# Performance work log

Hardware: AMD Instinct MI355X
Metric: run time of the kernel (lower is better)

Reference implementation:

```python
import jax, jax.numpy as jnp
import numpy as np
import itertools

N_INPUTS = 6
N_TERMS = 4
# static rule index table [R, n_inputs], R = n_terms ** n_inputs = 4096
RULE_IDX = np.array(list(itertools.product(range(N_TERMS), repeat=N_INPUTS)), dtype=np.int32)


def setup_inputs() -> dict:
    key = jax.random.key(0)
    k1, k2, k3, k4 = jax.random.split(key, 4)
    B = 32768
    x = jax.random.normal(k1, (B, N_INPUTS), dtype=jnp.float32)
    centers = jax.random.normal(k2, (N_INPUTS, N_TERMS), dtype=jnp.float32)
    sigmas = jax.random.uniform(k3, (N_INPUTS, N_TERMS), dtype=jnp.float32, minval=0.5, maxval=1.5)
    consequents = jax.random.normal(k4, (N_TERMS ** N_INPUTS, N_INPUTS + 1), dtype=jnp.float32)
    return {"x": x, "centers": centers, "sigmas": sigmas, "consequents": consequents}


def reference(x, centers, sigmas, consequents):
    # Gaussian memberships: mu[b, i, t]
    s = jnp.abs(sigmas) + 1e-6                          # [I, T]
    mu = jnp.exp(-((x[:, :, None] - centers[None]) ** 2) / (2.0 * s[None] ** 2))  # [B, I, T]
    # rule firing strengths: product over inputs of selected terms
    idx = jnp.asarray(RULE_IDX.T)                       # [I, R]
    mu_sel = jnp.take_along_axis(mu, idx[None], axis=2)  # [B, I, R]
    w = jnp.prod(mu_sel, axis=1)                        # [B, R]
    w_norm = w / (jnp.sum(w, axis=1, keepdims=True) + 1e-8)
    # consequent outputs: f[b, r] = [x, 1] @ consequents[r]
    x_aug = jnp.concatenate([x, jnp.ones((x.shape[0], 1), dtype=x.dtype)], axis=1)  # [B, I+1]
    f = x_aug @ consequents.T                           # [B, R]
    return jnp.sum(w_norm * f, axis=1, keepdims=True)   # [B, 1]
```

## Files before the change

### kernel.cpp

```cpp
#include <hip/hip_runtime.h>


typedef __attribute__((ext_vector_type(8))) short bf16x8;
typedef __attribute__((ext_vector_type(4))) float f32x4;

#define THREADS 256
#define BPB     64
#define PH_STR  66
#define PTT_STR 65

__device__ __forceinline__ unsigned int bf16rne(float f) {
    unsigned int u = __float_as_uint(f);
    u += 0x7fffu + ((u >> 16) & 1u);
    return u >> 16;
}

__global__ void anfis_prep(const float* __restrict__ cons, uint4* __restrict__ ws) {
    int id = blockIdx.x * blockDim.x + threadIdx.x;
    if (id >= 4096) return;
    int l = id >> 6, n = id & 63;
    const float* src = cons + (n * 64 + l) * 7;
    unsigned int h[8];
#pragma unroll
    for (int j = 0; j < 7; ++j) h[j] = bf16rne(src[j]);
    h[7] = 0;
    uint4 v;
    v.x = h[0] | (h[1] << 16);
    v.y = h[2] | (h[3] << 16);
    v.z = h[4] | (h[5] << 16);
    v.w = h[6] | (h[7] << 16);
    ws[id] = v;
}

__launch_bounds__(THREADS, 4)
__global__ void anfis_mfma(const float* __restrict__ x,
                           const float* __restrict__ centers,
                           const float* __restrict__ sigmas,
                           const uint4* __restrict__ wsC,
                           float* __restrict__ out, int B) {
    __shared__ float  PH[BPB * PH_STR];
    __shared__ float  PTT[64 * PTT_STR];
    __shared__ float4 xs4[BPB * 6 / 4];

    const int tid  = threadIdx.x;
    const int lane = tid & 63;
    const int wv   = tid >> 6;
    const long blockbase = (long)blockIdx.x * BPB;
    float* xs = (float*)xs4;

    if (lane < 24)
        xs4[wv * 24 + lane] = ((const float4*)x)[blockIdx.x * 96 + wv * 24 + lane];

    {
        const int d0 = (lane >> 4) & 3, d1 = (lane >> 2) & 3, d2 = lane & 3;
        const int t6[6] = {d0, d1, d2, d0, d1, d2};
        float cen[6], inv[6];
#pragma unroll
        for (int i = 0; i < 6; ++i) {
            cen[i] = centers[i * 4 + t6[i]];
            float s = fabsf(sigmas[i * 4 + t6[i]]) + 1e-6f;
            inv[i] = 0.5f / (s * s);
        }
#pragma unroll 4
        for (int g = 0; g < 16; ++g) {
            int bl = wv * 16 + g;
            float m[6];
#pragma unroll
            for (int i = 0; i < 6; ++i) {
                float d = xs[bl * 6 + i] - cen[i];
                m[i] = __expf(-d * d * inv[i]);
            }
            PH[bl * PH_STR + lane]   = m[0] * m[1] * m[2];
            PTT[lane * PTT_STR + bl] = m[3] * m[4] * m[5];
        }
    }

    const int t = lane & 15, q = lane >> 4, m0 = wv * 16;

    float xa[8];
#pragma unroll
    for (int j = 0; j < 6; ++j) xa[j] = xs[(m0 + t) * 6 + j];
    xa[6] = 1.f;
    xa[7] = 0.f;

    union U4 { unsigned int u[4]; bf16x8 v; };
    U4 B4;
    B4.u[0] = B4.u[1] = B4.u[2] = 0u;
    B4.u[3] = (t == 0) ? 0x00003f80u : 0u;

    f32x4 Dn[4], D4;
#pragma unroll
    for (int nt = 0; nt < 4; ++nt) Dn[nt] = (f32x4){0.f, 0.f, 0.f, 0.f};
    D4 = (f32x4){0.f, 0.f, 0.f, 0.f};

#pragma unroll 2
    for (int kt = 0; kt < 16; ++kt) {
        const int l = kt * 4 + q;
        U4 Bf[4];
#pragma unroll
        for (int nt = 0; nt < 4; ++nt) {
            uint4 bw = wsC[l * 64 + nt * 16 + t];
            Bf[nt].u[0] = bw.x; Bf[nt].u[1] = bw.y;
            Bf[nt].u[2] = bw.z; Bf[nt].u[3] = bw.w;
        }
        float ptv = PTT[l * PTT_STR + m0 + t];
        U4 Ah, Al;
#pragma unroll
        for (int jp = 0; jp < 4; ++jp) {
            float u0 = ptv * xa[2 * jp];
            float u1 = ptv * xa[2 * jp + 1];
            unsigned int b0 = __float_as_uint(u0), b1 = __float_as_uint(u1);
            unsigned int t0 = b0 & 0xffff0000u, t1 = b1 & 0xffff0000u;
            float l0 = u0 - __uint_as_float(t0);
            float l1 = u1 - __uint_as_float(t1);
            Ah.u[jp] = (b0 >> 16) | t1;
            Al.u[jp] = (__float_as_uint(l0) >> 16) | (__float_as_uint(l1) & 0xffff0000u);
        }
#pragma unroll
        for (int nt = 0; nt < 4; ++nt)
            Dn[nt] = __builtin_amdgcn_mfma_f32_16x16x32_bf16(Ah.v, Bf[nt].v, Dn[nt], 0, 0, 0);
        D4 = __builtin_amdgcn_mfma_f32_16x16x32_bf16(Ah.v, B4.v, D4, 0, 0, 0);
#pragma unroll
        for (int nt = 0; nt < 4; ++nt)
            Dn[nt] = __builtin_amdgcn_mfma_f32_16x16x32_bf16(Al.v, Bf[nt].v, Dn[nt], 0, 0, 0);
        D4 = __builtin_amdgcn_mfma_f32_16x16x32_bf16(Al.v, B4.v, D4, 0, 0, 0);
    }

    float Pn[4] = {0.f, 0.f, 0.f, 0.f};
    float Ps[4] = {0.f, 0.f, 0.f, 0.f};
    float Pd[4];
#pragma unroll
    for (int r = 0; r < 4; ++r) Pd[r] = D4[r];
#pragma unroll
    for (int nt = 0; nt < 4; ++nt)
#pragma unroll
        for (int r = 0; r < 4; ++r) {
            float phv = PH[(m0 + q * 4 + r) * PH_STR + nt * 16 + t];
            Pn[r] = fmaf(phv, Dn[nt][r], Pn[r]);
            Ps[r] += phv;
        }
#pragma unroll
    for (int off = 1; off < 16; off <<= 1)
#pragma unroll
        for (int r = 0; r < 4; ++r) {
            Pn[r] += __shfl_xor(Pn[r], off);
            Ps[r] += __shfl_xor(Ps[r], off);
            Pd[r] += __shfl_xor(Pd[r], off);
        }
    if (t == 0) {
        long bo = blockbase + m0 + q * 4;
        float o[4];
#pragma unroll
        for (int r = 0; r < 4; ++r) o[r] = Pn[r] / (Ps[r] * Pd[r] + 1e-8f);
        if (bo + 3 < B) {
            *(float4*)&out[bo] = make_float4(o[0], o[1], o[2], o[3]);
        } else {
#pragma unroll
            for (int r = 0; r < 4; ++r)
                if (bo + r < B) out[bo + r] = o[r];
        }
    }
}

extern "C" void kernel_launch(void* const* d_in, const int* in_sizes, int n_in,
                              void* d_out, int out_size, void* d_ws, size_t ws_size,
                              hipStream_t stream) {
    const float* x       = (const float*)d_in[0];
    const float* centers = (const float*)d_in[1];
    const float* sigmas  = (const float*)d_in[2];
    const float* cons    = (const float*)d_in[3];
    float* out = (float*)d_out;

    int B = in_sizes[0] / 6;
    uint4* wsC = (uint4*)d_ws;

    anfis_prep<<<16, 256, 0, stream>>>(cons, wsC);
    int blocks = (B + BPB - 1) / BPB;
    anfis_mfma<<<blocks, THREADS, 0, stream>>>(x, centers, sigmas, wsC, out, B);
}
```

Baseline: 69.82 us.

## Split K loop across wave pairs with shared-memory partial sum combine

Halves the batch rows per block and assigns two waves to each 16-row tile. Each wave of a pair computes half the membership products and half of the K loop, and the partial numerators and denominators are combined through shared memory. This doubles the number of blocks and splits per-wave MFMA work to improve latency hiding and occupancy. In exchange it adds two block-wide barriers, duplicates the B-fragment traffic per row, and adds a bounds-checked load for x.

New measurement: 69.91 us. About the same (+0.1%).

```diff
diff --git a/kernel.cpp b/kernel.cpp
--- a/kernel.cpp
+++ b/kernel.cpp
@@ -5,9 +5,9 @@
 typedef __attribute__((ext_vector_type(4))) float f32x4;
 
 #define THREADS 256
-#define BPB     64
+#define BPB     32
 #define PH_STR  66
-#define PTT_STR 65
+#define PTT_STR 33
 
 __device__ __forceinline__ unsigned int bf16rne(float f) {
     unsigned int u = __float_as_uint(f);
@@ -41,41 +41,51 @@
     __shared__ float  PH[BPB * PH_STR];
     __shared__ float  PTT[64 * PTT_STR];
     __shared__ float4 xs4[BPB * 6 / 4];
+    __shared__ float  comb[2 * 4 * 8];
 
     const int tid  = threadIdx.x;
     const int lane = tid & 63;
     const int wv   = tid >> 6;
+    const int pairid = wv >> 1;
+    const int half   = wv & 1;
     const long blockbase = (long)blockIdx.x * BPB;
     float* xs = (float*)xs4;
 
-    if (lane < 24)
-        xs4[wv * 24 + lane] = ((const float4*)x)[blockIdx.x * 96 + wv * 24 + lane];
+    if (lane < 24) {
+        long idx4 = (long)blockIdx.x * 48 + pairid * 24 + lane;
+        float4 v = (idx4 * 4 + 3 < (long)B * 6) ? ((const float4*)x)[idx4]
+                                                : make_float4(0.f, 0.f, 0.f, 0.f);
+        xs4[pairid * 24 + lane] = v;
+    }
 
     {
         const int d0 = (lane >> 4) & 3, d1 = (lane >> 2) & 3, d2 = lane & 3;
-        const int t6[6] = {d0, d1, d2, d0, d1, d2};
-        float cen[6], inv[6];
-#pragma unroll
-        for (int i = 0; i < 6; ++i) {
-            cen[i] = centers[i * 4 + t6[i]];
-            float s = fabsf(sigmas[i * 4 + t6[i]]) + 1e-6f;
+        const int ioff = half * 3;
+        const int t3[3] = {d0, d1, d2};
+        float cen[3], inv[3];
+#pragma unroll
+        for (int i = 0; i < 3; ++i) {
+            cen[i] = centers[(ioff + i) * 4 + t3[i]];
+            float s = fabsf(sigmas[(ioff + i) * 4 + t3[i]]) + 1e-6f;
             inv[i] = 0.5f / (s * s);
         }
 #pragma unroll 4
         for (int g = 0; g < 16; ++g) {
-            int bl = wv * 16 + g;
-            float m[6];
-#pragma unroll
-            for (int i = 0; i < 6; ++i) {
-                float d = xs[bl * 6 + i] - cen[i];
+            int bl = pairid * 16 + g;
+            float m[3];
+#pragma unroll
+            for (int i = 0; i < 3; ++i) {
+                float d = xs[bl * 6 + ioff + i] - cen[i];
                 m[i] = __expf(-d * d * inv[i]);
             }
-            PH[bl * PH_STR + lane]   = m[0] * m[1] * m[2];
-            PTT[lane * PTT_STR + bl] = m[3] * m[4] * m[5];
-        }
-    }
-
-    const int t = lane & 15, q = lane >> 4, m0 = wv * 16;
+            float prod = m[0] * m[1] * m[2];
+            if (half == 0) PH[bl * PH_STR + lane]   = prod;
+            else           PTT[lane * PTT_STR + bl] = prod;
+        }
+    }
+    __syncthreads();
+
+    const int t = lane & 15, q = lane >> 4, m0 = pairid * 16;
 
     float xa[8];
 #pragma unroll
@@ -93,9 +103,10 @@
     for (int nt = 0; nt < 4; ++nt) Dn[nt] = (f32x4){0.f, 0.f, 0.f, 0.f};
     D4 = (f32x4){0.f, 0.f, 0.f, 0.f};
 
-#pragma unroll 2
-    for (int kt = 0; kt < 16; ++kt) {
-        const int l = kt * 4 + q;
+#pragma unroll 4
+    for (int ktr = 0; ktr < 8; ++ktr) {
+        const int kt = half * 8 + ktr;
+        const int l  = kt * 4 + q;
         U4 Bf[4];
 #pragma unroll
         for (int nt = 0; nt < 4; ++nt) {
@@ -147,11 +158,23 @@
             Ps[r] += __shfl_xor(Ps[r], off);
             Pd[r] += __shfl_xor(Pd[r], off);
         }
-    if (t == 0) {
+    if (half == 1 && t == 0) {
+#pragma unroll
+        for (int r = 0; r < 4; ++r) {
+            comb[pairid * 32 + q * 8 + r]     = Pn[r];
+            comb[pairid * 32 + q * 8 + 4 + r] = Pd[r];
+        }
+    }
+    __syncthreads();
+    if (half == 0 && t == 0) {
         long bo = blockbase + m0 + q * 4;
         float o[4];
 #pragma unroll
-        for (int r = 0; r < 4; ++r) o[r] = Pn[r] / (Ps[r] * Pd[r] + 1e-8f);
+        for (int r = 0; r < 4; ++r) {
+            float n2 = Pn[r] + comb[pairid * 32 + q * 8 + r];
+            float d2 = Pd[r] + comb[pairid * 32 + q * 8 + 4 + r];
+            o[r] = n2 / (Ps[r] * d2 + 1e-8f);
+        }
         if (bo + 3 < B) {
             *(float4*)&out[bo] = make_float4(o[0], o[1], o[2], o[3]);
         } else {
```

## Fuse consequent prep into main kernel, compute memberships in registers, factor denominator

Applied to the files above, without the earlier changes.

Drops the separate prep kernel: every block now converts the consequent table to bf16 itself and keeps it in a large dynamic LDS table instead of reading it from a global workspace. Membership products are computed directly in registers per lane rather than staged through shared arrays. The normaliser is computed as a product of per-input membership sums, which removes the extra MFMA and the shuffle reductions that produced it. The cost is that each of the 512 blocks redundantly converts the 4096-row table, and the roughly 66KB of LDS limits occupancy to about 2 blocks per CU.

Measured after the change: 69.20 us. About the same (-0.9%).

```diff
diff --git a/kernel.cpp b/kernel.cpp
--- a/kernel.cpp
+++ b/kernel.cpp
@@ -5,9 +5,8 @@
 typedef __attribute__((ext_vector_type(4))) float f32x4;
 
 #define THREADS 256
-#define BPB     64
-#define PH_STR  66
-#define PTT_STR 65
+#define TAB_STR 65
+#define TAB_BYTES (64 * TAB_STR * 16)
 
 __device__ __forceinline__ unsigned int bf16rne(float f) {
     unsigned int u = __float_as_uint(f);
@@ -15,95 +14,136 @@
     return u >> 16;
 }
 
-__global__ void anfis_prep(const float* __restrict__ cons, uint4* __restrict__ ws) {
-    int id = blockIdx.x * blockDim.x + threadIdx.x;
-    if (id >= 4096) return;
-    int l = id >> 6, n = id & 63;
-    const float* src = cons + (n * 64 + l) * 7;
-    unsigned int h[8];
-#pragma unroll
-    for (int j = 0; j < 7; ++j) h[j] = bf16rne(src[j]);
-    h[7] = 0;
-    uint4 v;
-    v.x = h[0] | (h[1] << 16);
-    v.y = h[2] | (h[3] << 16);
-    v.z = h[4] | (h[5] << 16);
-    v.w = h[6] | (h[7] << 16);
-    ws[id] = v;
-}
-
-__launch_bounds__(THREADS, 4)
-__global__ void anfis_mfma(const float* __restrict__ x,
-                           const float* __restrict__ centers,
-                           const float* __restrict__ sigmas,
-                           const uint4* __restrict__ wsC,
-                           float* __restrict__ out, int B) {
-    __shared__ float  PH[BPB * PH_STR];
-    __shared__ float  PTT[64 * PTT_STR];
-    __shared__ float4 xs4[BPB * 6 / 4];
+__device__ __forceinline__ float sel4(float a0, float a1, float a2, float a3, int i) {
+    float lo = (i & 1) ? a1 : a0;
+    float hi = (i & 1) ? a3 : a2;
+    return (i & 2) ? hi : lo;
+}
+
+extern __shared__ uint4 tab[];
+
+__launch_bounds__(THREADS, 2)
+__global__ void anfis_one(const float* __restrict__ x,
+                          const float* __restrict__ centers,
+                          const float* __restrict__ sigmas,
+                          const float* __restrict__ cons,
+                          float* __restrict__ out, int B) {
+    __shared__ float4 xs4[96];
+    float* xs = (float*)xs4;
 
     const int tid  = threadIdx.x;
     const int lane = tid & 63;
     const int wv   = tid >> 6;
-    const long blockbase = (long)blockIdx.x * BPB;
-    float* xs = (float*)xs4;
-
-    if (lane < 24)
-        xs4[wv * 24 + lane] = ((const float4*)x)[blockIdx.x * 96 + wv * 24 + lane];
-
+    const long blockbase = (long)blockIdx.x * 64;
+
+    if (lane < 24) {
+        long i4 = (long)blockIdx.x * 96 + wv * 24 + lane;
+        float4 v = (i4 * 4 + 3 < (long)B * 6) ? ((const float4*)x)[i4]
+                                              : make_float4(0.f, 0.f, 0.f, 0.f);
+        xs4[wv * 24 + lane] = v;
+    }
+
+#pragma unroll 4
+    for (int i = 0; i < 16; ++i) {
+        int n = wv + 4 * i;
+        const float* src = cons + (n * 64 + lane) * 7;
+        unsigned int h0 = bf16rne(src[0]), h1 = bf16rne(src[1]);
+        unsigned int h2 = bf16rne(src[2]), h3 = bf16rne(src[3]);
+        unsigned int h4 = bf16rne(src[4]), h5 = bf16rne(src[5]);
+        unsigned int h6 = bf16rne(src[6]);
+        uint4 v;
+        v.x = h0 | (h1 << 16);
+        v.y = h2 | (h3 << 16);
+        v.z = h4 | (h5 << 16);
+        v.w = h6;
+        tab[lane * TAB_STR + n] = v;
+    }
+
+    const int t = lane & 15, q = lane >> 4;
+    const int lmA = wv * 16 + t;
+
+    float cenv[6][4], invv[6][4];
+#pragma unroll
+    for (int i = 0; i < 6; ++i)
+#pragma unroll
+        for (int tm = 0; tm < 4; ++tm) {
+            cenv[i][tm] = centers[i * 4 + tm];
+            float s = fabsf(sigmas[i * 4 + tm]) + 1e-6f;
+            invv[i][tm] = 0.5f / (s * s);
+        }
+
+    float xA[6];
+#pragma unroll
+    for (int j = 0; j < 6; ++j) xA[j] = xs[lmA * 6 + j];
+
+    float E[6][4];
+#pragma unroll
+    for (int i = 0; i < 6; ++i)
+#pragma unroll
+        for (int tm = 0; tm < 4; ++tm) {
+            float d = xA[i] - cenv[i][tm];
+            E[i][tm] = __expf(-d * d * invv[i][tm]);
+        }
+    float den_local = (E[0][0] + E[0][1] + E[0][2] + E[0][3])
+                    * (E[1][0] + E[1][1] + E[1][2] + E[1][3])
+                    * (E[2][0] + E[2][1] + E[2][2] + E[2][3])
+                    * (E[3][0] + E[3][1] + E[3][2] + E[3][3])
+                    * (E[4][0] + E[4][1] + E[4][2] + E[4][3])
+                    * (E[5][0] + E[5][1] + E[5][2] + E[5][3]);
+
+    float e5q = sel4(E[5][0], E[5][1], E[5][2], E[5][3], q);
+    float pt16[16];
+#pragma unroll
+    for (int kt = 0; kt < 16; ++kt)
+        pt16[kt] = E[3][kt >> 2] * E[4][kt & 3] * e5q;
+
+    float PH16[4][4];
     {
-        const int d0 = (lane >> 4) & 3, d1 = (lane >> 2) & 3, d2 = lane & 3;
-        const int t6[6] = {d0, d1, d2, d0, d1, d2};
-        float cen[6], inv[6];
-#pragma unroll
-        for (int i = 0; i < 6; ++i) {
-            cen[i] = centers[i * 4 + t6[i]];
-            float s = fabsf(sigmas[i * 4 + t6[i]]) + 1e-6f;
-            inv[i] = 0.5f / (s * s);
-        }
-#pragma unroll 4
-        for (int g = 0; g < 16; ++g) {
-            int bl = wv * 16 + g;
-            float m[6];
-#pragma unroll
-            for (int i = 0; i < 6; ++i) {
-                float d = xs[bl * 6 + i] - cen[i];
-                m[i] = __expf(-d * d * inv[i]);
+        const int tm1 = t >> 2, tm2 = t & 3;
+        float c1 = sel4(cenv[1][0], cenv[1][1], cenv[1][2], cenv[1][3], tm1);
+        float i1 = sel4(invv[1][0], invv[1][1], invv[1][2], invv[1][3], tm1);
+        float c2 = sel4(cenv[2][0], cenv[2][1], cenv[2][2], cenv[2][3], tm2);
+        float i2 = sel4(invv[2][0], invv[2][1], invv[2][2], invv[2][3], tm2);
+#pragma unroll
+        for (int r = 0; r < 4; ++r) {
+            int lr = wv * 16 + q * 4 + r;
+            float x0 = xs[lr * 6 + 0];
+            float x1 = xs[lr * 6 + 1];
+            float x2 = xs[lr * 6 + 2];
+            float d1 = x1 - c1, d2 = x2 - c2;
+            float G12 = __expf(-d1 * d1 * i1) * __expf(-d2 * d2 * i2);
+#pragma unroll
+            for (int nt = 0; nt < 4; ++nt) {
+                float d0 = x0 - cenv[0][nt];
+                PH16[r][nt] = G12 * __expf(-d0 * d0 * invv[0][nt]);
             }
-            PH[bl * PH_STR + lane]   = m[0] * m[1] * m[2];
-            PTT[lane * PTT_STR + bl] = m[3] * m[4] * m[5];
-        }
-    }
-
-    const int t = lane & 15, q = lane >> 4, m0 = wv * 16;
+        }
+    }
 
     float xa[8];
 #pragma unroll
-    for (int j = 0; j < 6; ++j) xa[j] = xs[(m0 + t) * 6 + j];
+    for (int j = 0; j < 6; ++j) xa[j] = xA[j];
     xa[6] = 1.f;
     xa[7] = 0.f;
 
+    __syncthreads();
+
     union U4 { unsigned int u[4]; bf16x8 v; };
-    U4 B4;
-    B4.u[0] = B4.u[1] = B4.u[2] = 0u;
-    B4.u[3] = (t == 0) ? 0x00003f80u : 0u;
-
-    f32x4 Dn[4], D4;
+    f32x4 Dn[4];
 #pragma unroll
     for (int nt = 0; nt < 4; ++nt) Dn[nt] = (f32x4){0.f, 0.f, 0.f, 0.f};
-    D4 = (f32x4){0.f, 0.f, 0.f, 0.f};
-
-#pragma unroll 2
+
+#pragma unroll 4
     for (int kt = 0; kt < 16; ++kt) {
-        const int l = kt * 4 + q;
+        const uint4* base = &tab[(kt * 4 + q) * TAB_STR + t];
         U4 Bf[4];
 #pragma unroll
         for (int nt = 0; nt < 4; ++nt) {
-            uint4 bw = wsC[l * 64 + nt * 16 + t];
+            uint4 bw = base[nt * 16];
             Bf[nt].u[0] = bw.x; Bf[nt].u[1] = bw.y;
             Bf[nt].u[2] = bw.z; Bf[nt].u[3] = bw.w;
         }
-        float ptv = PTT[l * PTT_STR + m0 + t];
+        float ptv = pt16[kt];
         U4 Ah, Al;
 #pragma unroll
         for (int jp = 0; jp < 4; ++jp) {
@@ -119,39 +159,33 @@
 #pragma unroll
         for (int nt = 0; nt < 4; ++nt)
             Dn[nt] = __builtin_amdgcn_mfma_f32_16x16x32_bf16(Ah.v, Bf[nt].v, Dn[nt], 0, 0, 0);
-        D4 = __builtin_amdgcn_mfma_f32_16x16x32_bf16(Ah.v, B4.v, D4, 0, 0, 0);
 #pragma unroll
         for (int nt = 0; nt < 4; ++nt)
             Dn[nt] = __builtin_amdgcn_mfma_f32_16x16x32_bf16(Al.v, Bf[nt].v, Dn[nt], 0, 0, 0);
-        D4 = __builtin_amdgcn_mfma_f32_16x16x32_bf16(Al.v, B4.v, D4, 0, 0, 0);
     }
 
     float Pn[4] = {0.f, 0.f, 0.f, 0.f};
-    float Ps[4] = {0.f, 0.f, 0.f, 0.f};
-    float Pd[4];
-#pragma unroll
-    for (int r = 0; r < 4; ++r) Pd[r] = D4[r];
 #pragma unroll
     for (int nt = 0; nt < 4; ++nt)
 #pragma unroll
-        for (int r = 0; r < 4; ++r) {
-            float phv = PH[(m0 + q * 4 + r) * PH_STR + nt * 16 + t];
-            Pn[r] = fmaf(phv, Dn[nt][r], Pn[r]);
-            Ps[r] += phv;
-        }
+        for (int r = 0; r < 4; ++r)
+            Pn[r] = fmaf(PH16[r][nt], Dn[nt][r], Pn[r]);
 #pragma unroll
     for (int off = 1; off < 16; off <<= 1)
 #pragma unroll
-        for (int r = 0; r < 4; ++r) {
+        for (int r = 0; r < 4; ++r)
             Pn[r] += __shfl_xor(Pn[r], off);
-            Ps[r] += __shfl_xor(Ps[r], off);
-            Pd[r] += __shfl_xor(Pd[r], off);
-        }
+
+    float dq[4];
+#pragma unroll
+    for (int r = 0; r < 4; ++r)
+        dq[r] = __shfl(den_local, q * 4 + r);
+
     if (t == 0) {
-        long bo = blockbase + m0 + q * 4;
+        long bo = blockbase + wv * 16 + q * 4;
         float o[4];
 #pragma unroll
-        for (int r = 0; r < 4; ++r) o[r] = Pn[r] / (Ps[r] * Pd[r] + 1e-8f);
+        for (int r = 0; r < 4; ++r) o[r] = Pn[r] / (dq[r] + 1e-8f);
         if (bo + 3 < B) {
             *(float4*)&out[bo] = make_float4(o[0], o[1], o[2], o[3]);
         } else {
@@ -172,9 +206,9 @@
     float* out = (float*)d_out;
 
     int B = in_sizes[0] / 6;
-    uint4* wsC = (uint4*)d_ws;
-
-    anfis_prep<<<16, 256, 0, stream>>>(cons, wsC);
-    int blocks = (B + BPB - 1) / BPB;
-    anfis_mfma<<<blocks, THREADS, 0, stream>>>(x, centers, sigmas, wsC, out, B);
-}
+    hipFuncSetAttribute(reinterpret_cast<const void*>(anfis_one),
+                        hipFuncAttributeMaxDynamicSharedMemorySize, TAB_BYTES);
+    int blocks = (B + 63) / 64;
+    anfis_one<<<blocks, THREADS, TAB_BYTES, stream>>>(x, centers, sigmas, cons,
+                                                      out, B);
+}
```
